# Kernel optimization log

Measured on AMD Instinct MI355X. Metric: run time of the kernel, lower is better.

## Reference

```python
import jax, jax.numpy as jnp
import numpy as np

B, S, HID = 4, 2048, 576
NH, NKV, HD = 9, 3, 64
MAXPOS, THETA = 8192, 100000.0


def rotate_half(x):
    x1, x2 = x[..., : x.shape[-1] // 2], x[..., x.shape[-1] // 2 :]
    return jnp.concatenate((-x2, x1), axis=-1)


def setup_inputs() -> dict:
    key = jax.random.key(0)
    ks = jax.random.split(key, 6)
    x = jax.random.normal(ks[0], (B, S, HID), dtype=jnp.float32)
    # RoPE tables (HuggingFace layout: freqs duplicated across halves)
    inv_freq = 1.0 / (THETA ** (np.arange(0, HD, 2, dtype=np.float32) / HD))
    freqs = np.outer(np.arange(MAXPOS, dtype=np.float32), inv_freq)
    emb = np.concatenate([freqs, freqs], axis=-1)
    cos = jnp.asarray(np.cos(emb))
    sin = jnp.asarray(np.sin(emb))
    position_ids = jnp.broadcast_to(jnp.arange(S, dtype=jnp.int64), (B, S))
    # additive causal mask [B,1,S,S]
    causal = jnp.where(
        jnp.tril(jnp.ones((S, S), dtype=bool)), 0.0, -1e9
    ).astype(jnp.float32)
    attention_mask = jnp.broadcast_to(causal, (B, 1, S, S))
    scale = 0.02
    wq = jax.random.normal(ks[1], (NH * HD, HID), dtype=jnp.float32) * scale
    wk = jax.random.normal(ks[2], (NKV * HD, HID), dtype=jnp.float32) * scale
    wv = jax.random.normal(ks[3], (NKV * HD, HID), dtype=jnp.float32) * scale
    wo = jax.random.normal(ks[4], (HID, NH * HD), dtype=jnp.float32) * scale
    return {
        "x": x, "cos": cos, "sin": sin, "position_ids": position_ids,
        "attention_mask": attention_mask,
        "wq": wq, "wk": wk, "wv": wv, "wo": wo,
    }


def reference(x, cos, sin, position_ids, attention_mask, wq, wk, wv, wo):
    b, s, _ = x.shape
    # projections (nn.Linear: y = x @ W.T), split into heads -> [B,H,S,D]
    q = (x @ wq.T).reshape(b, s, NH, HD).transpose(0, 2, 1, 3)
    k = (x @ wk.T).reshape(b, s, NKV, HD).transpose(0, 2, 1, 3)
    v = (x @ wv.T).reshape(b, s, NKV, HD).transpose(0, 2, 1, 3)
    # RoPE: cos/sin gathered per position -> [B,1,S,D], broadcast over heads
    c = cos[position_ids][:, None, :, :]
    si = sin[position_ids][:, None, :, :]
    q = q * c + rotate_half(q) * si
    k = k * c + rotate_half(k) * si
    # GQA expansion: repeat_interleave kv heads to match q heads
    k = jnp.repeat(k, NH // NKV, axis=1)
    v = jnp.repeat(v, NH // NKV, axis=1)
    scale = 1.0 / jnp.sqrt(jnp.asarray(HD, dtype=x.dtype))
    scores = jnp.einsum("bhqd,bhkd->bhqk", q, k) * scale + attention_mask
    attn = jax.nn.softmax(scores.astype(jnp.float32), axis=-1).astype(q.dtype)
    out = jnp.einsum("bhqk,bhkd->bhqd", attn, v)
    out = out.transpose(0, 2, 1, 3).reshape(b, s, NH * HD)
    return out @ wo.T
```

## Files before the change

### kernel.cpp

```cpp
#include <hip/hip_runtime.h>
#include <hip/hip_bf16.h>

#define B_    4
#define S_    2048
#define HID_  576
#define NH_   9
#define NKV_  3
#define HD_   64
#define GQ_   3

typedef __attribute__((ext_vector_type(8))) short bf16x8;
typedef __attribute__((ext_vector_type(4))) float f32x4;

__device__ __forceinline__ short f2bf(float f) {
    union { float f; unsigned int u; } v; v.f = f;
    unsigned int r = (v.u + 0x7fffu + ((v.u >> 16) & 1u)) >> 16;
    return (short)r;
}

__device__ __forceinline__ float exp2fast(float x) {
    return __builtin_amdgcn_exp2f(x);
}

__device__ __forceinline__ void async16(const void* g, void* l) {
    __builtin_amdgcn_global_load_lds(
        (const __attribute__((address_space(1))) unsigned int*)g,
        (__attribute__((address_space(3))) unsigned int*)l, 16, 0, 0);
}

#define NX_   (8192 * 576)
#define NWQ_  (576 * 576)
#define NWK_  (192 * 576)
#define NWV_  (192 * 576)
#define NWO_  (576 * 576)
#define NTOT_ (NX_ + NWQ_ + NWK_ + NWV_ + NWO_)

__global__ __launch_bounds__(256) void convert_kernel(
    const float* __restrict__ x,  const float* __restrict__ wq,
    const float* __restrict__ wk, const float* __restrict__ wv,
    const float* __restrict__ wo,
    short* __restrict__ xb, short* __restrict__ wqkvb, short* __restrict__ wob)
{
    int i4 = (blockIdx.x * 256 + threadIdx.x) * 4;
    const float* src; short* dst;
    if (i4 < NX_)                          { src = x  + i4;                          dst = xb    + i4; }
    else if (i4 < NX_ + NWQ_)              { src = wq + (i4 - NX_);                  dst = wqkvb + (i4 - NX_); }
    else if (i4 < NX_ + NWQ_ + NWK_)       { src = wk + (i4 - NX_ - NWQ_);           dst = wqkvb + (i4 - NX_); }
    else if (i4 < NX_ + NWQ_ + NWK_ + NWV_){ src = wv + (i4 - NX_ - NWQ_ - NWK_);    dst = wqkvb + (i4 - NX_); }
    else                                   { src = wo + (i4 - NX_ - NWQ_ - NWK_ - NWV_);
                                             dst = wob + (i4 - NX_ - NWQ_ - NWK_ - NWV_); }
    float4 v = *(const float4*)src;
    short4 o = make_short4(f2bf(v.x), f2bf(v.y), f2bf(v.z), f2bf(v.w));
    *(short4*)dst = o;
}

__global__ __launch_bounds__(256) void qkv_kernel(
    const short* __restrict__ xb,
    const short* __restrict__ wqkvb,
    const float* __restrict__ cosb,
    const float* __restrict__ sinb,
    short* __restrict__ Q,
    short* __restrict__ K,
    short* __restrict__ Vt)
{
    __shared__ __align__(16) short As[2][256 * 64];
    __shared__ __align__(16) short Bs[2][64 * 64];

    const int m0     = blockIdx.x * 256;
    const int nb_blk = blockIdx.y;
    const int tid  = threadIdx.x;
    const int w    = tid >> 6, lane = tid & 63;
    const int quad = lane >> 4, c = lane & 15;
    const int lr   = lane >> 3, lg = lane & 7;
    const int sw   = lg ^ lr;
    const int xg   = quad ^ (c & 7);

    auto stage = [&](int step, short* dstA, short* dstB) {
        const int k0 = step * 64;
        #pragma unroll
        for (int r = 0; r < 8; ++r) {
            int ch = w * 8 + r, R = ch * 8 + lr;
            async16(xb + (size_t)(m0 + R) * HID_ + k0 + sw * 8, (char*)dstA + ch * 1024);
        }
        #pragma unroll
        for (int r = 0; r < 2; ++r) {
            int ch = w * 2 + r, R = ch * 8 + lr;
            async16(wqkvb + (size_t)(nb_blk * 64 + R) * HID_ + k0 + sw * 8, (char*)dstB + ch * 1024);
        }
    };

    f32x4 acc[4][4];
    #pragma unroll
    for (int mt = 0; mt < 4; ++mt)
        #pragma unroll
        for (int nb = 0; nb < 4; ++nb) acc[mt][nb] = (f32x4){0.f, 0.f, 0.f, 0.f};

    stage(0, As[0], Bs[0]);

    int buf = 0;
    for (int kk = 0; kk < 9; ++kk) {
        __syncthreads();
        if (kk < 8) stage(kk + 1, As[buf ^ 1], Bs[buf ^ 1]);

        const short* a_s = As[buf];
        const short* b_s = Bs[buf];
        bf16x8 bfr[4][2];
        #pragma unroll
        for (int nb = 0; nb < 4; ++nb) {
            int row = nb * 16 + c;
            bfr[nb][0] = *(const bf16x8*)(b_s + row * 64 + xg * 8);
            bfr[nb][1] = *(const bf16x8*)(b_s + row * 64 + (xg ^ 4) * 8);
        }
        #pragma unroll
        for (int mt = 0; mt < 4; ++mt) {
            int row = w * 64 + mt * 16 + c;
            bf16x8 a0 = *(const bf16x8*)(a_s + row * 64 + xg * 8);
            bf16x8 a1 = *(const bf16x8*)(a_s + row * 64 + (xg ^ 4) * 8);
            #pragma unroll
            for (int nb = 0; nb < 4; ++nb) {
                acc[mt][nb] = __builtin_amdgcn_mfma_f32_16x16x32_bf16(a0, bfr[nb][0], acc[mt][nb], 0, 0, 0);
                acc[mt][nb] = __builtin_amdgcn_mfma_f32_16x16x32_bf16(a1, bfr[nb][1], acc[mt][nb], 0, 0, 0);
            }
        }
        buf ^= 1;
    }

    int type, head;
    if (nb_blk < NH_)            { type = 0; head = nb_blk; }
    else if (nb_blk < NH_ + NKV_){ type = 1; head = nb_blk - NH_; }
    else                         { type = 2; head = nb_blk - NH_ - NKV_; }
    const int b  = m0 >> 11;
    const int s0 = m0 & (S_ - 1);

    if (type < 2) {
        const float qs = (type == 0) ? 0.18033688f : 1.0f;
        #pragma unroll
        for (int mt = 0; mt < 4; ++mt)
            #pragma unroll
            for (int reg = 0; reg < 4; ++reg) {
                int s = s0 + w * 64 + mt * 16 + quad * 4 + reg;
                const float* cr = cosb + (size_t)s * HD_;
                const float* sr = sinb + (size_t)s * HD_;
                float a0 = acc[mt][0][reg], a1 = acc[mt][1][reg];
                float a2 = acc[mt][2][reg], a3 = acc[mt][3][reg];
                float o0 = (a0 * cr[c]      - a2 * sr[c])      * qs;
                float o1 = (a1 * cr[c + 16] - a3 * sr[c + 16]) * qs;
                float o2 = (a2 * cr[c + 32] + a0 * sr[c + 32]) * qs;
                float o3 = (a3 * cr[c + 48] + a1 * sr[c + 48]) * qs;
                short* dst = (type == 0)
                    ? Q + (((size_t)b * NH_  + head) * S_ + s) * HD_
                    : K + (((size_t)b * NKV_ + head) * S_ + s) * HD_;
                dst[c]      = f2bf(o0);
                dst[c + 16] = f2bf(o1);
                dst[c + 32] = f2bf(o2);
                dst[c + 48] = f2bf(o3);
            }
    } else {
        short* base = Vt + (((size_t)b * NKV_ + head) * HD_) * S_;
        #pragma unroll
        for (int mt = 0; mt < 4; ++mt) {
            int s4 = s0 + w * 64 + mt * 16 + quad * 4;
            #pragma unroll
            for (int nb = 0; nb < 4; ++nb) {
                int d = nb * 16 + c;
                short4 pk = make_short4(f2bf(acc[mt][nb][0]), f2bf(acc[mt][nb][1]),
                                        f2bf(acc[mt][nb][2]), f2bf(acc[mt][nb][3]));
                *(short4*)(base + (size_t)d * S_ + s4) = pk;
            }
        }
    }
}

#define PSTR 72

__global__ __launch_bounds__(256) void attn_kernel(
    const short* __restrict__ Q,
    const short* __restrict__ K,
    const short* __restrict__ Vt,
    short* __restrict__ AOb)
{
    __shared__ __align__(16) short Qs[64 * 64];
    __shared__ __align__(16) short Ks[2][64 * 64];
    __shared__ __align__(16) short Vs[2][64 * 64];
    __shared__ __align__(16) short Ps[64 * PSTR];

    const int hb = blockIdx.x;
    const int h  = hb >> 2, b = hb & 3;
    const int qt = 31 - blockIdx.y;
    const int kh = h / GQ_;
    const int tid  = threadIdx.x;
    const int w    = tid >> 6, lane = tid & 63;
    const int quad = lane >> 4, c = lane & 15;
    const int lr   = lane >> 3, lg = lane & 7;
    const int sw   = lg ^ lr;
    const int xg   = quad ^ (c & 7);

    const short* Qg = Q  + (((size_t)b * NH_  + h ) * S_ + qt * 64) * HD_;
    const short* Kg = K  + (((size_t)b * NKV_ + kh) * S_) * HD_;
    const short* Vg = Vt + (((size_t)b * NKV_ + kh) * HD_) * S_;

    #pragma unroll
    for (int r = 0; r < 2; ++r) {
        int ch = w * 2 + r, R = ch * 8 + lr;
        async16(Qg + (size_t)R * HD_ + sw * 8, (char*)Qs + ch * 1024);
    }
    #pragma unroll
    for (int r = 0; r < 4; ++r) {
        int it = w * 4 + r;
        if (it < 8) {
            int R = it * 8 + lr;
            async16(Kg + (size_t)R * HD_ + sw * 8, (char*)Ks[0] + it * 1024);
        } else {
            int R = (it - 8) * 8 + lr;
            async16(Vg + (size_t)R * S_ + sw * 8, (char*)Vs[0] + (it - 8) * 1024);
        }
    }

    bf16x8 ones;
    #pragma unroll
    for (int i = 0; i < 8; ++i) ones[i] = (short)0x3F80;

    f32x4 acc_o[4];
    #pragma unroll
    for (int nb = 0; nb < 4; ++nb) acc_o[nb] = (f32x4){0.f, 0.f, 0.f, 0.f};
    f32x4 acc_l = (f32x4){0.f, 0.f, 0.f, 0.f};

    bf16x8 aq0, aq1;

    auto do_tile = [&](const short* ks, const short* vs, bool MASK) {
        f32x4 sc[4];
        #pragma unroll
        for (int nb = 0; nb < 4; ++nb) {
            bf16x8 bk0 = *(const bf16x8*)(ks + (nb * 16 + c) * 64 + xg * 8);
            bf16x8 bk1 = *(const bf16x8*)(ks + (nb * 16 + c) * 64 + (xg ^ 4) * 8);
            f32x4 z = (f32x4){0.f, 0.f, 0.f, 0.f};
            z = __builtin_amdgcn_mfma_f32_16x16x32_bf16(aq0, bk0, z, 0, 0, 0);
            z = __builtin_amdgcn_mfma_f32_16x16x32_bf16(aq1, bk1, z, 0, 0, 0);
            sc[nb] = z;
        }
        #pragma unroll
        for (int r = 0; r < 4; ++r) {
            const int qrow = w * 16 + quad * 4 + r;
            #pragma unroll
            for (int nb = 0; nb < 4; ++nb) {
                float sv = sc[nb][r] - 4.0f;
                if (MASK && (nb * 16 + c > qrow)) sv = -1e30f;
                Ps[(w * 16 + quad * 4 + r) * PSTR + nb * 16 + c] = f2bf(exp2fast(sv));
            }
        }
        #pragma unroll
        for (int kc = 0; kc < 2; ++kc) {
            bf16x8 ap = *(const bf16x8*)(Ps + (w * 16 + c) * PSTR + quad * 8 + kc * 32);
            int pg = kc ? (xg ^ 4) : xg;
            #pragma unroll
            for (int nb = 0; nb < 4; ++nb) {
                bf16x8 bv = *(const bf16x8*)(vs + (nb * 16 + c) * 64 + pg * 8);
                acc_o[nb] = __builtin_amdgcn_mfma_f32_16x16x32_bf16(ap, bv, acc_o[nb], 0, 0, 0);
            }
            acc_l = __builtin_amdgcn_mfma_f32_16x16x32_bf16(ap, ones, acc_l, 0, 0, 0);
        }
    };

    __syncthreads();
    aq0 = *(const bf16x8*)(Qs + (w * 16 + c) * 64 + xg * 8);
    aq1 = *(const bf16x8*)(Qs + (w * 16 + c) * 64 + (xg ^ 4) * 8);

    int buf = 0;
    for (int kt = 0; kt < qt; ++kt) {
        int nxt = buf ^ 1;
        #pragma unroll
        for (int r = 0; r < 4; ++r) {
            int it = w * 4 + r;
            if (it < 8) {
                int R = it * 8 + lr;
                async16(Kg + (size_t)((kt + 1) * 64 + R) * HD_ + sw * 8,
                        (char*)Ks[nxt] + it * 1024);
            } else {
                int R = (it - 8) * 8 + lr;
                async16(Vg + (size_t)R * S_ + (kt + 1) * 64 + sw * 8,
                        (char*)Vs[nxt] + (it - 8) * 1024);
            }
        }
        do_tile(Ks[buf], Vs[buf], false);
        __syncthreads();
        buf ^= 1;
    }
    do_tile(Ks[buf], Vs[buf], true);

    #pragma unroll
    for (int r = 0; r < 4; ++r) {
        int s = qt * 64 + w * 16 + quad * 4 + r;
        float inv = 1.f / acc_l[r];
        short* dst = AOb + (((size_t)b * S_ + s) * NH_ + h) * HD_;
        #pragma unroll
        for (int nb = 0; nb < 4; ++nb)
            dst[nb * 16 + c] = f2bf(acc_o[nb][r] * inv);
    }
}

__global__ __launch_bounds__(256) void oproj_kernel(
    const short* __restrict__ AOb,
    const short* __restrict__ wob,
    float* __restrict__ out)
{
    __shared__ __align__(16) short As[2][256 * 64];
    __shared__ __align__(16) short Bs[2][64 * 64];

    const int m0 = blockIdx.x * 256;
    const int n0 = blockIdx.y * 64;
    const int tid  = threadIdx.x;
    const int w    = tid >> 6, lane = tid & 63;
    const int quad = lane >> 4, c = lane & 15;
    const int lr   = lane >> 3, lg = lane & 7;
    const int sw   = lg ^ lr;
    const int xg   = quad ^ (c & 7);

    auto stage = [&](int step, short* dstA, short* dstB) {
        const int k0 = step * 64;
        #pragma unroll
        for (int r = 0; r < 8; ++r) {
            int ch = w * 8 + r, R = ch * 8 + lr;
            async16(AOb + (size_t)(m0 + R) * HID_ + k0 + sw * 8, (char*)dstA + ch * 1024);
        }
        #pragma unroll
        for (int r = 0; r < 2; ++r) {
            int ch = w * 2 + r, R = ch * 8 + lr;
            async16(wob + (size_t)(n0 + R) * HID_ + k0 + sw * 8, (char*)dstB + ch * 1024);
        }
    };

    f32x4 acc[4][4];
    #pragma unroll
    for (int mt = 0; mt < 4; ++mt)
        #pragma unroll
        for (int nb = 0; nb < 4; ++nb) acc[mt][nb] = (f32x4){0.f, 0.f, 0.f, 0.f};

    stage(0, As[0], Bs[0]);

    int buf = 0;
    for (int kk = 0; kk < 9; ++kk) {
        __syncthreads();
        if (kk < 8) stage(kk + 1, As[buf ^ 1], Bs[buf ^ 1]);

        const short* a_s = As[buf];
        const short* b_s = Bs[buf];
        bf16x8 bfr[4][2];
        #pragma unroll
        for (int nb = 0; nb < 4; ++nb) {
            int row = nb * 16 + c;
            bfr[nb][0] = *(const bf16x8*)(b_s + row * 64 + xg * 8);
            bfr[nb][1] = *(const bf16x8*)(b_s + row * 64 + (xg ^ 4) * 8);
        }
        #pragma unroll
        for (int mt = 0; mt < 4; ++mt) {
            int row = w * 64 + mt * 16 + c;
            bf16x8 a0 = *(const bf16x8*)(a_s + row * 64 + xg * 8);
            bf16x8 a1 = *(const bf16x8*)(a_s + row * 64 + (xg ^ 4) * 8);
            #pragma unroll
            for (int nb = 0; nb < 4; ++nb) {
                acc[mt][nb] = __builtin_amdgcn_mfma_f32_16x16x32_bf16(a0, bfr[nb][0], acc[mt][nb], 0, 0, 0);
                acc[mt][nb] = __builtin_amdgcn_mfma_f32_16x16x32_bf16(a1, bfr[nb][1], acc[mt][nb], 0, 0, 0);
            }
        }
        buf ^= 1;
    }

    #pragma unroll
    for (int mt = 0; mt < 4; ++mt)
        #pragma unroll
        for (int reg = 0; reg < 4; ++reg) {
            int m = m0 + w * 64 + mt * 16 + quad * 4 + reg;
            float* dst = out + (size_t)m * HID_ + n0;
            #pragma unroll
            for (int nb = 0; nb < 4; ++nb)
                dst[nb * 16 + c] = acc[mt][nb][reg];
        }
}

extern "C" void kernel_launch(void* const* d_in, const int* in_sizes, int n_in,
                              void* d_out, int out_size, void* d_ws, size_t ws_size,
                              hipStream_t stream) {
    const float* x    = (const float*)d_in[0];
    const float* cosb = (const float*)d_in[1];
    const float* sinb = (const float*)d_in[2];
    const float* wq   = (const float*)d_in[5];
    const float* wk   = (const float*)d_in[6];
    const float* wv   = (const float*)d_in[7];
    const float* wo   = (const float*)d_in[8];

    short* xb    = (short*)d_ws;
    short* wqkvb = xb    + (size_t)NX_;
    short* wob   = wqkvb + (size_t)(NWQ_ + NWK_ + NWV_);
    short* Qb    = wob   + (size_t)NWO_;
    short* Kb    = Qb    + (size_t)B_ * NH_  * S_ * HD_;
    short* Vtb   = Kb    + (size_t)B_ * NKV_ * S_ * HD_;
    short* AOb   = Vtb   + (size_t)B_ * NKV_ * S_ * HD_;

    convert_kernel<<<dim3(NTOT_ / 4 / 256), dim3(256), 0, stream>>>(
        x, wq, wk, wv, wo, xb, wqkvb, wob);
    qkv_kernel<<<dim3(32, 15), dim3(256), 0, stream>>>(
        xb, wqkvb, cosb, sinb, Qb, Kb, Vtb);
    attn_kernel<<<dim3(36, 32), dim3(256), 0, stream>>>(Qb, Kb, Vtb, AOb);
    oproj_kernel<<<dim3(32, 9), dim3(256), 0, stream>>>(AOb, wob, (float*)d_out);
}
```

Measured before the change: 191.7 us.

## Pair causal query tiles per block and remap grids for XCD-local L2 reuse

The attention kernel now processes two query tiles per block (qt=31-y and qt=y), so every block does the same amount of causal work and the grid shrinks to 576 blocks. All three GEMM/attention kernels switch to a 1D grid with a (bid&7)-based remap, so that blocks sharing K/V or weight tiles land on the same XCD and reuse its L2. Both changes target load imbalance in the causal loop and cross-XCD cache misses. In exchange, each attention block runs twice as long in sequence and adds extra syncs between its two halves.

```diff
diff --git a/kernel.cpp b/kernel.cpp
--- a/kernel.cpp
+++ b/kernel.cpp
@@ -66,8 +66,10 @@
     __shared__ __align__(16) short As[2][256 * 64];
     __shared__ __align__(16) short Bs[2][64 * 64];
 
-    const int m0     = blockIdx.x * 256;
-    const int nb_blk = blockIdx.y;
+    const int bid = blockIdx.x;
+    const int f   = (bid & 7) * 60 + (bid >> 3);
+    const int m0     = (f / 15) * 256;
+    const int nb_blk = f % 15;
     const int tid  = threadIdx.x;
     const int w    = tid >> 6, lane = tid & 63;
     const int quad = lane >> 4, c = lane & 15;
@@ -184,10 +186,13 @@
     __shared__ __align__(16) short Vs[2][64 * 64];
     __shared__ __align__(16) short Ps[64 * PSTR];
 
-    const int hb = blockIdx.x;
-    const int h  = hb >> 2, b = hb & 3;
-    const int qt = 31 - blockIdx.y;
-    const int kh = h / GQ_;
+    const int bid = blockIdx.x;
+    const int f   = (bid & 7) * 72 + (bid >> 3);
+    const int g   = f / 48, u = f % 48;
+    const int b   = g & 3, kh = g >> 2;
+    const int h   = kh * GQ_ + u / 16;
+    const int y   = u % 16;
+
     const int tid  = threadIdx.x;
     const int w    = tid >> 6, lane = tid & 63;
     const int quad = lane >> 4, c = lane & 15;
@@ -195,36 +200,15 @@
     const int sw   = lg ^ lr;
     const int xg   = quad ^ (c & 7);
 
-    const short* Qg = Q  + (((size_t)b * NH_  + h ) * S_ + qt * 64) * HD_;
     const short* Kg = K  + (((size_t)b * NKV_ + kh) * S_) * HD_;
     const short* Vg = Vt + (((size_t)b * NKV_ + kh) * HD_) * S_;
-
-    #pragma unroll
-    for (int r = 0; r < 2; ++r) {
-        int ch = w * 2 + r, R = ch * 8 + lr;
-        async16(Qg + (size_t)R * HD_ + sw * 8, (char*)Qs + ch * 1024);
-    }
-    #pragma unroll
-    for (int r = 0; r < 4; ++r) {
-        int it = w * 4 + r;
-        if (it < 8) {
-            int R = it * 8 + lr;
-            async16(Kg + (size_t)R * HD_ + sw * 8, (char*)Ks[0] + it * 1024);
-        } else {
-            int R = (it - 8) * 8 + lr;
-            async16(Vg + (size_t)R * S_ + sw * 8, (char*)Vs[0] + (it - 8) * 1024);
-        }
-    }
 
     bf16x8 ones;
     #pragma unroll
     for (int i = 0; i < 8; ++i) ones[i] = (short)0x3F80;
 
     f32x4 acc_o[4];
-    #pragma unroll
-    for (int nb = 0; nb < 4; ++nb) acc_o[nb] = (f32x4){0.f, 0.f, 0.f, 0.f};
-    f32x4 acc_l = (f32x4){0.f, 0.f, 0.f, 0.f};
-
+    f32x4 acc_l;
     bf16x8 aq0, aq1;
 
     auto do_tile = [&](const short* ks, const short* vs, bool MASK) {
@@ -261,41 +245,70 @@
         }
     };
 
-    __syncthreads();
-    aq0 = *(const bf16x8*)(Qs + (w * 16 + c) * 64 + xg * 8);
-    aq1 = *(const bf16x8*)(Qs + (w * 16 + c) * 64 + (xg ^ 4) * 8);
-
-    int buf = 0;
-    for (int kt = 0; kt < qt; ++kt) {
-        int nxt = buf ^ 1;
+    auto run_half = [&](int qt) {
+        const short* Qg = Q + (((size_t)b * NH_ + h) * S_ + qt * 64) * HD_;
+
+        #pragma unroll
+        for (int r = 0; r < 2; ++r) {
+            int ch = w * 2 + r, R = ch * 8 + lr;
+            async16(Qg + (size_t)R * HD_ + sw * 8, (char*)Qs + ch * 1024);
+        }
         #pragma unroll
         for (int r = 0; r < 4; ++r) {
             int it = w * 4 + r;
             if (it < 8) {
                 int R = it * 8 + lr;
-                async16(Kg + (size_t)((kt + 1) * 64 + R) * HD_ + sw * 8,
-                        (char*)Ks[nxt] + it * 1024);
+                async16(Kg + (size_t)R * HD_ + sw * 8, (char*)Ks[0] + it * 1024);
             } else {
                 int R = (it - 8) * 8 + lr;
-                async16(Vg + (size_t)R * S_ + (kt + 1) * 64 + sw * 8,
-                        (char*)Vs[nxt] + (it - 8) * 1024);
-            }
-        }
-        do_tile(Ks[buf], Vs[buf], false);
+                async16(Vg + (size_t)R * S_ + sw * 8, (char*)Vs[0] + (it - 8) * 1024);
+            }
+        }
+
+        #pragma unroll
+        for (int nb = 0; nb < 4; ++nb) acc_o[nb] = (f32x4){0.f, 0.f, 0.f, 0.f};
+        acc_l = (f32x4){0.f, 0.f, 0.f, 0.f};
+
         __syncthreads();
-        buf ^= 1;
-    }
-    do_tile(Ks[buf], Vs[buf], true);
-
-    #pragma unroll
-    for (int r = 0; r < 4; ++r) {
-        int s = qt * 64 + w * 16 + quad * 4 + r;
-        float inv = 1.f / acc_l[r];
-        short* dst = AOb + (((size_t)b * S_ + s) * NH_ + h) * HD_;
-        #pragma unroll
-        for (int nb = 0; nb < 4; ++nb)
-            dst[nb * 16 + c] = f2bf(acc_o[nb][r] * inv);
-    }
+        aq0 = *(const bf16x8*)(Qs + (w * 16 + c) * 64 + xg * 8);
+        aq1 = *(const bf16x8*)(Qs + (w * 16 + c) * 64 + (xg ^ 4) * 8);
+
+        int buf = 0;
+        for (int kt = 0; kt < qt; ++kt) {
+            int nxt = buf ^ 1;
+            #pragma unroll
+            for (int r = 0; r < 4; ++r) {
+                int it = w * 4 + r;
+                if (it < 8) {
+                    int R = it * 8 + lr;
+                    async16(Kg + (size_t)((kt + 1) * 64 + R) * HD_ + sw * 8,
+                            (char*)Ks[nxt] + it * 1024);
+                } else {
+                    int R = (it - 8) * 8 + lr;
+                    async16(Vg + (size_t)R * S_ + (kt + 1) * 64 + sw * 8,
+                            (char*)Vs[nxt] + (it - 8) * 1024);
+                }
+            }
+            do_tile(Ks[buf], Vs[buf], false);
+            __syncthreads();
+            buf ^= 1;
+        }
+        do_tile(Ks[buf], Vs[buf], true);
+
+        #pragma unroll
+        for (int r = 0; r < 4; ++r) {
+            int s = qt * 64 + w * 16 + quad * 4 + r;
+            float inv = 1.f / acc_l[r];
+            short* dst = AOb + (((size_t)b * S_ + s) * NH_ + h) * HD_;
+            #pragma unroll
+            for (int nb = 0; nb < 4; ++nb)
+                dst[nb * 16 + c] = f2bf(acc_o[nb][r] * inv);
+        }
+        __syncthreads();
+    };
+
+    run_half(31 - y);
+    run_half(y);
 }
 
 __global__ __launch_bounds__(256) void oproj_kernel(
@@ -306,8 +319,10 @@
     __shared__ __align__(16) short As[2][256 * 64];
     __shared__ __align__(16) short Bs[2][64 * 64];
 
-    const int m0 = blockIdx.x * 256;
-    const int n0 = blockIdx.y * 64;
+    const int bid = blockIdx.x;
+    const int f   = (bid & 7) * 36 + (bid >> 3);
+    const int m0 = (f / 9) * 256;
+    const int n0 = (f % 9) * 64;
     const int tid  = threadIdx.x;
     const int w    = tid >> 6, lane = tid & 63;
     const int quad = lane >> 4, c = lane & 15;
@@ -398,8 +413,8 @@
 
     convert_kernel<<<dim3(NTOT_ / 4 / 256), dim3(256), 0, stream>>>(
         x, wq, wk, wv, wo, xb, wqkvb, wob);
-    qkv_kernel<<<dim3(32, 15), dim3(256), 0, stream>>>(
+    qkv_kernel<<<dim3(480), dim3(256), 0, stream>>>(
         xb, wqkvb, cosb, sinb, Qb, Kb, Vtb);
-    attn_kernel<<<dim3(36, 32), dim3(256), 0, stream>>>(Qb, Kb, Vtb, AOb);
-    oproj_kernel<<<dim3(32, 9), dim3(256), 0, stream>>>(AOb, wob, (float*)d_out);
-}
+    attn_kernel<<<dim3(576), dim3(256), 0, stream>>>(Qb, Kb, Vtb, AOb);
+    oproj_kernel<<<dim3(288), dim3(256), 0, stream>>>(AOb, wob, (float*)d_out);
+}
```

Result: slower. 201.9 us (+5.4%).
